# Kernel tuning notes

Measured on AMD Instinct MI355X. Metric: run time of the kernel, lower is better.

Reference implementation:

```python
import jax, jax.numpy as jnp
import numpy as np
from jax import lax

CUT = 20            # voxel grid per side, hard-coded in the torch module
N, P, OP = 32, 8192, 2048


def _w(key, shape, fan_in):
    return jax.random.normal(key, shape, dtype=jnp.float32) * np.float32(1.0 / np.sqrt(fan_in))


def setup_inputs() -> dict:
    key = jax.random.key(0)
    ks = jax.random.split(key, 20)
    inp = {}
    inp["sc"] = jax.random.uniform(ks[0], (N, P, 2), dtype=jnp.float32, minval=-0.5, maxval=0.5)
    inp["oc"] = jax.random.uniform(ks[1], (N, OP, 2), dtype=jnp.float32, minval=-0.5, maxval=0.5)
    inp["pos"] = jax.random.uniform(ks[2], (N, 2), dtype=jnp.float32, minval=-0.5, maxval=0.5)
    # voxel PointNet MLP (1x1 Conv1d == per-point linear)
    inp["mlp_w1"] = _w(ks[3], (128, 2), 2);        inp["mlp_b1"] = jnp.zeros((128,), jnp.float32)
    inp["mlp_w2"] = _w(ks[4], (256, 128), 128);    inp["mlp_b2"] = jnp.zeros((256,), jnp.float32)
    # dense conv pyramid
    inp["conv1_w"] = _w(ks[5], (512, 256, 3, 3), 256 * 9);   inp["conv1_b"] = jnp.zeros((512,), jnp.float32)
    inp["conv2_w"] = _w(ks[6], (1024, 512, 3, 3), 512 * 9);  inp["conv2_b"] = jnp.zeros((1024,), jnp.float32)
    inp["convt_w"] = _w(ks[7], (512, 1024, 2, 2), 1024 * 4); inp["convt_b"] = jnp.zeros((512,), jnp.float32)
    # object set-abstraction (stack of 1x1 Conv1d)
    inp["sa_w1"] = _w(ks[8], (64, 2), 2);          inp["sa_b1"] = jnp.zeros((64,), jnp.float32)
    inp["sa_w2"] = _w(ks[9], (128, 64), 64);       inp["sa_b2"] = jnp.zeros((128,), jnp.float32)
    inp["sa_w3"] = _w(ks[10], (256, 128), 128);    inp["sa_b3"] = jnp.zeros((256,), jnp.float32)
    inp["sa_w4"] = _w(ks[11], (512, 256), 256);    inp["sa_b4"] = jnp.zeros((512,), jnp.float32)
    # per-cell classifier
    inp["cls_w1"] = _w(ks[12], (1024, 1538), 1538); inp["cls_b1"] = jnp.zeros((1024,), jnp.float32)
    inp["cls_w2"] = _w(ks[13], (256, 1024), 1024);  inp["cls_b2"] = jnp.zeros((256,), jnp.float32)
    inp["cls_w3"] = _w(ks[14], (1, 256), 256);      inp["cls_b3"] = jnp.zeros((1,), jnp.float32)
    return inp


def _conv2d(x, w, b):
    y = lax.conv_general_dilated(x, w, (1, 1), ((1, 1), (1, 1)),
                                 dimension_numbers=("NCHW", "OIHW", "NCHW"))
    return y + b[None, :, None, None]


def _maxpool2(x):
    return lax.reduce_window(x, -jnp.inf, lax.max, (1, 1, 2, 2), (1, 1, 2, 2), "VALID")


def reference(sc, oc, pos,
              mlp_w1, mlp_b1, mlp_w2, mlp_b2,
              conv1_w, conv1_b, conv2_w, conv2_b, convt_w, convt_b,
              sa_w1, sa_b1, sa_w2, sa_b2, sa_w3, sa_b3, sa_w4, sa_b4,
              cls_w1, cls_b1, cls_w2, cls_b2, cls_w3, cls_b3):
    n = sc.shape[0]
    # ---- fused voxelization + PointNet + scatter-max (replaces triple loop) ----
    x, y = sc[..., 0], sc[..., 1]
    # torch condition: cut[i] < x <= cut[i+1] on linspace(-0.5, 0.5, 21)
    bi = jnp.clip(jnp.ceil((x + 0.5) * CUT) - 1, 0, CUT - 1).astype(jnp.int32)
    bj = jnp.clip(jnp.ceil((y + 0.5) * CUT) - 1, 0, CUT - 1).astype(jnp.int32)
    valid = (x > -0.5) & (x <= 0.5) & (y > -0.5) & (y <= 0.5)
    ci = -0.5 + (bi.astype(sc.dtype) + 0.5) / CUT   # voxel center x
    cj = -0.5 + (bj.astype(sc.dtype) + 0.5) / CUT   # voxel center y
    pc = jnp.stack([x - ci, y - cj], axis=-1).reshape(-1, 2)        # [n*P, 2]
    h = jax.nn.relu(pc @ mlp_w1.T + mlp_b1)
    feat = jax.nn.relu(h @ mlp_w2.T + mlp_b2)                       # [n*P, 256]
    seg = jnp.where(valid,
                    jnp.arange(n, dtype=jnp.int32)[:, None] * (CUT * CUT) + bi * CUT + bj,
                    n * CUT * CUT).reshape(-1)                      # invalid -> dummy bin
    nseg = n * CUT * CUT + 1
    mx = jax.ops.segment_max(feat, seg, num_segments=nseg)
    cnt = jax.ops.segment_sum(jnp.ones((n * P,), jnp.float32), seg, num_segments=nseg)
    vox = jnp.where(cnt[:, None] > 0, mx, 0.0)[: n * CUT * CUT]     # empty voxels stay 0
    vox = vox.reshape(n, CUT, CUT, 256).transpose(0, 3, 1, 2)       # [n,256,20,20]
    # ---- dense conv pyramid ----
    f1 = _maxpool2(jax.nn.relu(_conv2d(vox, conv1_w, conv1_b)))     # [n,512,10,10]
    f2 = _maxpool2(jax.nn.relu(_conv2d(f1, conv2_w, conv2_b)))      # [n,1024,5,5]
    f3 = lax.conv_transpose(f2, convt_w, (2, 2), "VALID",
                            dimension_numbers=("NCHW", "OIHW", "NCHW"))
    f3 = f3 + convt_b[None, :, None, None]                          # [n,512,10,10]
    scene = jnp.concatenate([f1, f3], axis=1)                       # [n,1024,10,10]
    S = scene.shape[2]
    scene_flat = scene.reshape(n, 1024, S * S)
    # ---- object PointNet (1x1 convs == per-point linears) + global max ----
    obj_c = oc - jnp.mean(oc, axis=1, keepdims=True)                # [n,OP,2]
    g = jax.nn.relu(obj_c @ sa_w1.T + sa_b1)
    g = jax.nn.relu(g @ sa_w2.T + sa_b2)
    g = jax.nn.relu(g @ sa_w3.T + sa_b3)
    g = jax.nn.relu(g @ sa_w4.T + sa_b4)                            # [n,OP,512]
    obj = jnp.max(g, axis=1)                                        # [n,512]
    obj_tiled = jnp.broadcast_to(obj[:, :, None], (n, 512, S * S))
    # ---- relative position grid ----
    c = -0.5 + (jnp.arange(S, dtype=sc.dtype) + 0.5) / S
    rel_x = jnp.broadcast_to(pos[:, 0][:, None, None] - c[None, :, None], (n, S, S))
    rel_y = jnp.broadcast_to(pos[:, 1][:, None, None] - c[None, None, :], (n, S, S))
    rel = jnp.stack([rel_x, rel_y], axis=1).reshape(n, 2, S * S)
    # ---- per-cell classifier ----
    cin = jnp.concatenate([scene_flat, obj_tiled, rel], axis=1).transpose(0, 2, 1)  # [n,100,1538]
    h = jax.nn.relu(cin @ cls_w1.T + cls_b1)
    h = jax.nn.relu(h @ cls_w2.T + cls_b2)
    return h @ cls_w3.T + cls_b3                                    # [n,100,1]
```

## Files before the change

### kernel.cpp

```cpp
#include <hip/hip_runtime.h>

#define NB 32
#define PP 8192
#define OPP 2048

typedef _Float16 f16;
typedef f16 half8 __attribute__((ext_vector_type(8)));
typedef f16 half4 __attribute__((ext_vector_type(4)));
typedef f16 half2v __attribute__((ext_vector_type(2)));
typedef float f32x4 __attribute__((ext_vector_type(4)));

#define MFMA16(a, b, c) __builtin_amdgcn_mfma_f32_16x16x32_f16(a, b, c, 0, 0, 0)

__global__ __launch_bounds__(256) void prepfuse_k(
    const float* __restrict__ mlp_w2, const float* __restrict__ sa_w2,
    const float* __restrict__ sa_w3, const float* __restrict__ sa_w4,
    const float* __restrict__ cls_w2, const float* __restrict__ cls_w1,
    const float* __restrict__ convt_w, const float* __restrict__ conv1_w,
    const float* __restrict__ conv2_w, const float* __restrict__ oc,
    f16* __restrict__ mw2h, f16* __restrict__ saw2h, f16* __restrict__ saw3h,
    f16* __restrict__ saw4h, f16* __restrict__ cw2h, f16* __restrict__ cw1h,
    f16* __restrict__ ctwh, f16* __restrict__ w1h, f16* __restrict__ w2h,
    float* __restrict__ ocm) {
  __shared__ float tile[512 * 9];
  int bb = blockIdx.x, t = threadIdx.x;
  if (bb < 2048) {
    constexpr int B0 = 8192, B1 = B0 + 2048, B2 = B1 + 8192, B3 = B2 + 32768, B4 = B3 + 65536;
    constexpr int C1e = B4 + 524288;
    constexpr int TOT = C1e + 2097152;
    for (int idx = bb * 256 + t; idx < TOT; idx += 2048 * 256) {
      if (idx < B4) {
        const float* in; f16* out; int off;
        if (idx < B0)      { in = mlp_w2; out = mw2h;  off = idx; }
        else if (idx < B1) { in = sa_w2;  out = saw2h; off = idx - B0; }
        else if (idx < B2) { in = sa_w3;  out = saw3h; off = idx - B1; }
        else if (idx < B3) { in = sa_w4;  out = saw4h; off = idx - B2; }
        else               { in = cls_w2; out = cw2h;  off = idx - B3; }
        float4 v = ((const float4*)in)[off];
        half4 h; h.x = (f16)v.x; h.y = (f16)v.y; h.z = (f16)v.z; h.w = (f16)v.w;
        ((half4*)out)[off] = h;
      } else if (idx < C1e) {
        int i = idx - B4;
        int co = i >> 9, k2 = i & 511;
        float2 v = *(const float2*)(cls_w1 + (size_t)co * 1538 + k2 * 2);
        half2v h = {(f16)v.x, (f16)v.y};
        *(half2v*)(cw1h + (size_t)co * 1024 + k2 * 2) = h;
      } else {
        int i = idx - C1e;
        int j = i & 7, l = (i >> 3) & 63, kb = (i >> 9) & 31, nb = i >> 14;
        int n16 = l & 15, quad = l >> 4;
        int np = nb * 16 + n16;
        int k = kb * 32 + quad * 8 + j;
        int p = np >> 9, o = np & 511;
        ctwh[i] = (f16)convt_w[((size_t)o * 1024 + k) * 4 + (3 - p)];
      }
    }
  } else if (bb < 2080) {
    float* sx = tile; float* sy = tile + 256;
    int n = bb - 2048;
    float ax = 0.f, ay = 0.f;
    for (int p = t; p < OPP; p += 256) {
      ax += oc[((size_t)n * OPP + p) * 2 + 0];
      ay += oc[((size_t)n * OPP + p) * 2 + 1];
    }
    sx[t] = ax; sy[t] = ay;
    __syncthreads();
    for (int s = 128; s > 0; s >>= 1) {
      if (t < s) { sx[t] += sx[t + s]; sy[t] += sy[t + s]; }
      __syncthreads();
    }
    if (t == 0) {
      ocm[n * 2 + 0] = sx[0] / (float)OPP;
      ocm[n * 2 + 1] = sy[0] / (float)OPP;
    }
  } else {
    int co, CI, NBB; const float* src0; f16* wf;
    if (bb < 2592) { co = bb - 2080; CI = 256; NBB = 32; src0 = conv1_w; wf = w1h; }
    else           { co = bb - 2592; CI = 512; NBB = 64; src0 = conv2_w; wf = w2h; }
    const float* src = src0 + (size_t)co * CI * 9;
    for (int i = t; i < CI * 9; i += 256) tile[i] = src[i];
    __syncthreads();
    int nb = co >> 4, l16c = co & 15;
    int tot = (CI / 32) * 9 * 4;
    for (int e = t; e < tot; e += 256) {
      int quad = e & 3;
      int kk = (e >> 2) % 9;
      int cic = e / 36;
      half8 v;
#pragma unroll
      for (int j = 0; j < 8; ++j) v[j] = (f16)tile[(cic * 32 + quad * 8 + j) * 9 + kk];
      *(half8*)(wf + ((((size_t)cic * 9 + kk) * NBB + nb) * 64 + quad * 16 + l16c) * 8) = v;
    }
  }
}

__global__ void cvt16_k(const float* __restrict__ in, f16* __restrict__ out, int n4) {
  int idx = blockIdx.x * 256 + threadIdx.x;
  if (idx >= n4) return;
  float4 v = ((const float4*)in)[idx];
  half4 h; h.x = (f16)v.x; h.y = (f16)v.y; h.z = (f16)v.z; h.w = (f16)v.w;
  ((half4*)out)[idx] = h;
}

__global__ __launch_bounds__(256) void pointnet_lds_k(
    const float* __restrict__ sc, const float* __restrict__ w1, const float* __restrict__ b1,
    const f16* __restrict__ w2h, const float* __restrict__ b2, float* __restrict__ voxg) {
  __shared__ float voxl[400 * 33];
  int t = threadIdx.x, lane = t & 63, w = t >> 6;
  int quad = lane >> 4, l16 = lane & 15;
  int b = blockIdx.x;
  int ps = b & 3, cg = (b >> 2) & 7, n = b >> 5;
  half2v w1x2[16], w1y2[16], b12[16];
#pragma unroll
  for (int i = 0; i < 16; ++i) {
    int k0 = (i >> 2) * 32 + quad * 8 + (i & 3) * 2;
    w1x2[i] = (half2v){(f16)w1[k0 * 2], (f16)w1[(k0 + 1) * 2]};
    w1y2[i] = (half2v){(f16)w1[k0 * 2 + 1], (f16)w1[(k0 + 1) * 2 + 1]};
    b12[i]  = (half2v){(f16)b1[k0], (f16)b1[k0 + 1]};
  }
  half8 bf[2][4];
  float bias[2];
#pragma unroll
  for (int nt = 0; nt < 2; ++nt) {
    int ch = cg * 32 + nt * 16 + l16;
    bias[nt] = b2[ch];
#pragma unroll
    for (int ks = 0; ks < 4; ++ks)
      bf[nt][ks] = *(const half8*)(w2h + (size_t)ch * 128 + ks * 32 + quad * 8);
  }
  for (int i = t; i < 400 * 33; i += 256) voxl[i] = 0.0f;
  __syncthreads();
  const half2v z2 = {};
  const float* scp = sc + ((size_t)n * PP + (size_t)ps * 2048) * 2;
  int p0 = w * 16 + l16;
  float2 xyA = *(const float2*)(scp + p0 * 2);
  float2 xyB = *(const float2*)(scp + (p0 + 64) * 2);
  for (int it = 0; it < 16; ++it) {
    float xA = xyA.x, yA = xyA.y, xB = xyB.x, yB = xyB.y;
    if (it < 15) {
      xyA = *(const float2*)(scp + ((it + 1) * 128 + p0) * 2);
      xyB = *(const float2*)(scp + ((it + 1) * 128 + p0 + 64) * 2);
    }
    float bifA = fminf(fmaxf(ceilf((xA + 0.5f) * 20.0f) - 1.0f, 0.0f), 19.0f);
    float bjfA = fminf(fmaxf(ceilf((yA + 0.5f) * 20.0f) - 1.0f, 0.0f), 19.0f);
    bool vA = (xA > -0.5f) && (xA <= 0.5f) && (yA > -0.5f) && (yA <= 0.5f);
    float pxA = xA - (-0.5f + (bifA + 0.5f) * 0.05f);
    float pyA = yA - (-0.5f + (bjfA + 0.5f) * 0.05f);
    int bnA = vA ? ((int)bifA * 20 + (int)bjfA) : -1;
    float bifB = fminf(fmaxf(ceilf((xB + 0.5f) * 20.0f) - 1.0f, 0.0f), 19.0f);
    float bjfB = fminf(fmaxf(ceilf((yB + 0.5f) * 20.0f) - 1.0f, 0.0f), 19.0f);
    bool vB = (xB > -0.5f) && (xB <= 0.5f) && (yB > -0.5f) && (yB <= 0.5f);
    float pxB = xB - (-0.5f + (bifB + 0.5f) * 0.05f);
    float pyB = yB - (-0.5f + (bjfB + 0.5f) * 0.05f);
    int bnB = vB ? ((int)bifB * 20 + (int)bjfB) : -1;
    f16 pxhA = (f16)pxA, pyhA = (f16)pyA, pxhB = (f16)pxB, pyhB = (f16)pyB;
    half2v px2A = (half2v){pxhA, pxhA}, py2A = (half2v){pyhA, pyhA};
    half2v px2B = (half2v){pxhB, pxhB}, py2B = (half2v){pyhB, pyhB};
    f32x4 acc0A = {}, acc1A = {}, acc0B = {}, acc1B = {};
#pragma unroll
    for (int ks = 0; ks < 4; ++ks) {
      half8 afA, afB;
#pragma unroll
      for (int j2 = 0; j2 < 4; ++j2) {
        half2v wx = w1x2[ks * 4 + j2], wy = w1y2[ks * 4 + j2], bb = b12[ks * 4 + j2];
        half2v tA = wx * px2A + (wy * py2A + bb);
        half2v tB = wx * px2B + (wy * py2B + bb);
        reinterpret_cast<half2v*>(&afA)[j2] = __builtin_elementwise_max(tA, z2);
        reinterpret_cast<half2v*>(&afB)[j2] = __builtin_elementwise_max(tB, z2);
      }
      acc0A = MFMA16(afA, bf[0][ks], acc0A);
      acc0B = MFMA16(afB, bf[0][ks], acc0B);
      acc1A = MFMA16(afA, bf[1][ks], acc1A);
      acc1B = MFMA16(afB, bf[1][ks], acc1B);
    }
#pragma unroll
    for (int r = 0; r < 4; ++r) {
      int bnA2 = __shfl(bnA, quad * 4 + r);
      int bnB2 = __shfl(bnB, quad * 4 + r);
      if (bnA2 >= 0) {
        float v0 = fmaxf(acc0A[r] + bias[0], 0.0f);
        float v1 = fmaxf(acc1A[r] + bias[1], 0.0f);
        atomicMax((int*)voxl + bnA2 * 33 + l16, __float_as_int(v0));
        atomicMax((int*)voxl + bnA2 * 33 + 16 + l16, __float_as_int(v1));
      }
      if (bnB2 >= 0) {
        float v0 = fmaxf(acc0B[r] + bias[0], 0.0f);
        float v1 = fmaxf(acc1B[r] + bias[1], 0.0f);
        atomicMax((int*)voxl + bnB2 * 33 + l16, __float_as_int(v0));
        atomicMax((int*)voxl + bnB2 * 33 + 16 + l16, __float_as_int(v1));
      }
    }
  }
  __syncthreads();
  float* vg = voxg + ((size_t)n * 400) * 256 + cg * 32;
  for (int i = t; i < 400 * 32; i += 256) {
    int bin = i >> 5, c = i & 31;
    float v = voxl[bin * 33 + c];
    if (v > 0.0f)
      atomicMax((int*)(vg + (size_t)bin * 256) + c, __float_as_int(v));
  }
}

template <int H, int W, int CI, int CO, int MSPLIT>
__global__ __launch_bounds__(256, 2) void convmfma_k(
    const f16* __restrict__ inh, const f16* __restrict__ wf,
    const float* __restrict__ bias, f16* __restrict__ outh) {
  constexpr int HS = H / MSPLIT;
  constexpr int Mpix = HS * W;
  constexpr int MT = (Mpix + 15) / 16;
  constexpr int PR = HS + 2, PC = W + 2;
  constexpr int NCIC = CI / 32;
  constexpr int COG = CO / 128;
  constexpr int NBB = CO / 16;
  extern __shared__ char smem[];
  f16* Ap = (f16*)smem;
  int b = blockIdx.x;
  int cog = b % COG;
  int ms = (b / COG) % MSPLIT;
  int n = b / (COG * MSPLIT);
  int co0 = cog * 128;
  int r0 = ms * HS;
  int t = threadIdx.x, lane = t & 63, w = t >> 6;
  int quad = lane >> 4, l16 = lane & 15;
  int nb0 = cog * 8 + w * 2;

  int abase[MT];
#pragma unroll
  for (int mi = 0; mi < MT; ++mi) {
    int pl = mi * 16 + l16; if (pl > Mpix - 1) pl = Mpix - 1;
    int y = pl / W, x = pl - y * W;
    abase[mi] = (y * PC + x) * 40 + quad * 8;
  }
  f32x4 acc[MT][2] = {};

  const f16* inbase = inh + (size_t)n * H * W * CI;

  for (int cic = 0; cic < NCIC; ++cic) {
    __syncthreads();
    for (int cell = t; cell < PR * PC; cell += 256) {
      int pr = cell / PC, pc = cell - pr * PC;
      int yin = r0 - 1 + pr, xin = pc - 1;
      uint4 d0 = {0,0,0,0}, d1 = {0,0,0,0}, d2 = {0,0,0,0}, d3 = {0,0,0,0};
      if (yin >= 0 && yin < H && xin >= 0 && xin < W) {
        const uint4* src = (const uint4*)(inbase + ((size_t)yin * W + xin) * CI + cic * 32);
        d0 = src[0]; d1 = src[1]; d2 = src[2]; d3 = src[3];
      }
      uint4* dst = (uint4*)(Ap + cell * 40);
      dst[0] = d0; dst[1] = d1; dst[2] = d2; dst[3] = d3;
    }
    __syncthreads();
    const f16* wfc = wf + (size_t)(cic * 9) * NBB * 512;
#pragma unroll
    for (int ky = 0; ky < 3; ++ky)
#pragma unroll
      for (int kx = 0; kx < 3; ++kx) {
        int kk = ky * 3 + kx;
        half8 bf0 = *(const half8*)(wfc + ((size_t)(kk * NBB + nb0) * 64 + lane) * 8);
        half8 bf1 = *(const half8*)(wfc + ((size_t)(kk * NBB + nb0 + 1) * 64 + lane) * 8);
        int shift = (ky * PC + kx) * 40;
#pragma unroll
        for (int mi = 0; mi < MT; ++mi) {
          half8 af = *(const half8*)(Ap + abase[mi] + shift);
          acc[mi][0] = MFMA16(af, bf0, acc[mi][0]);
          acc[mi][1] = MFMA16(af, bf1, acc[mi][1]);
        }
      }
  }
  int co_w = co0 + w * 32;
  float bv0 = bias[co_w + l16];
  float bv1 = bias[co_w + 16 + l16];
  f16* ob = outh + ((size_t)n * H * W + (size_t)ms * Mpix) * CO;
#pragma unroll
  for (int mi = 0; mi < MT; ++mi) {
#pragma unroll
    for (int r = 0; r < 4; ++r) {
      int p = mi * 16 + quad * 4 + r;
      if (p < Mpix) {
        float v0 = acc[mi][0][r] + bv0; v0 = v0 > 0.f ? v0 : 0.f;
        float v1 = acc[mi][1][r] + bv1; v1 = v1 > 0.f ? v1 : 0.f;
        ob[(size_t)p * CO + co_w + l16] = (f16)v0;
        ob[(size_t)p * CO + co_w + 16 + l16] = (f16)v1;
      }
    }
  }
}

__global__ void pool1_k(const f16* __restrict__ g1, f16* __restrict__ f1h,
                        f16* __restrict__ scnh) {
  int idx = blockIdx.x * 256 + threadIdx.x;
  if (idx >= 32 * 100 * 256) return;
  int c2 = idx & 255, rem = idx >> 8;
  int op = rem % 100, n = rem / 100;
  int py = op / 10, px = op - py * 10;
  const f16* base = g1 + (((size_t)n * 400 + (size_t)(2 * py) * 20 + 2 * px) * 512) + c2 * 2;
  float a0 = (float)base[0],   a1 = (float)base[1];
  float b0 = (float)base[512], b1 = (float)base[513];
  const f16* base2 = base + 20 * 512;
  float c0 = (float)base2[0],   c1 = (float)base2[1];
  float d0 = (float)base2[512], d1 = (float)base2[513];
  union { f16 h[2]; unsigned u; } pk;
  pk.h[0] = (f16)fmaxf(fmaxf(a0, b0), fmaxf(c0, d0));
  pk.h[1] = (f16)fmaxf(fmaxf(a1, b1), fmaxf(c1, d1));
  *(unsigned*)(f1h + ((size_t)n * 100 + op) * 512 + c2 * 2) = pk.u;
  *(unsigned*)(scnh + ((size_t)n * 100 + op) * 1024 + c2 * 2) = pk.u;
}

__global__ void pool2_k(const f16* __restrict__ g2, f16* __restrict__ f2h) {
  int idx = blockIdx.x * 256 + threadIdx.x;
  if (idx >= 32 * 25 * 512) return;
  int c2 = idx & 511, rem = idx >> 9;
  int op = rem % 25, n = rem / 25;
  int py = op / 5, px = op - py * 5;
  const f16* base = g2 + (((size_t)n * 100 + (size_t)(2 * py) * 10 + 2 * px) * 1024) + c2 * 2;
  float a0 = (float)base[0],    a1 = (float)base[1];
  float b0 = (float)base[1024], b1 = (float)base[1025];
  const f16* base2 = base + 10 * 1024;
  float c0 = (float)base2[0],    c1 = (float)base2[1];
  float d0 = (float)base2[1024], d1 = (float)base2[1025];
  f16* o = f2h + ((size_t)n * 25 + op) * 1024 + c2 * 2;
  o[0] = (f16)fmaxf(fmaxf(a0, b0), fmaxf(c0, d0));
  o[1] = (f16)fmaxf(fmaxf(a1, b1), fmaxf(c1, d1));
}

__global__ __launch_bounds__(256, 2) void convt_mfma_k(
    const f16* __restrict__ f2h, const f16* __restrict__ ctwf,
    const float* __restrict__ ctb, f16* __restrict__ scnh) {
  __shared__ f16 act[25 * 1048];
  int b = blockIdx.x;
  int ng = b & 15, n = b >> 4;
  int t = threadIdx.x, lane = t & 63, w = t >> 6;
  int quad = lane >> 4, l16 = lane & 15;
  for (int i = t; i < 25 * 128; i += 256) {
    int row = i >> 7, c8 = i & 127;
    *(half8*)(act + row * 1048 + c8 * 8) =
        *(const half8*)(f2h + ((size_t)n * 25 + row) * 1024 + c8 * 8);
  }
  __syncthreads();
  int r1 = 16 + (l16 > 8 ? 8 : l16);
  f32x4 acc[2][2] = {};
  const f16* wp0 = ctwf + ((size_t)((ng * 8 + w * 2 + 0) * 32) * 64 + lane) * 8;
  const f16* wp1 = ctwf + ((size_t)((ng * 8 + w * 2 + 1) * 32) * 64 + lane) * 8;
#pragma unroll 4
  for (int ks = 0; ks < 32; ++ks) {
    half8 a0 = *(const half8*)(act + l16 * 1048 + ks * 32 + quad * 8);
    half8 a1 = *(const half8*)(act + r1 * 1048 + ks * 32 + quad * 8);
    half8 b0 = *(const half8*)(wp0 + (size_t)ks * 512);
    half8 b1 = *(const half8*)(wp1 + (size_t)ks * 512);
    acc[0][0] = MFMA16(a0, b0, acc[0][0]);
    acc[1][0] = MFMA16(a1, b0, acc[1][0]);
    acc[0][1] = MFMA16(a0, b1, acc[0][1]);
    acc[1][1] = MFMA16(a1, b1, acc[1][1]);
  }
#pragma unroll
  for (int nt = 0; nt < 2; ++nt) {
    int np = ng * 128 + w * 32 + nt * 16 + l16;
    int p = np >> 9, co = np & 511;
    int a = p >> 1, bc = p & 1;
    float bb = ctb[co];
#pragma unroll
    for (int mt = 0; mt < 2; ++mt)
#pragma unroll
      for (int r = 0; r < 4; ++r) {
        int px = mt * 16 + quad * 4 + r;
        if (px < 25) {
          int ph = px / 5, pw = px - ph * 5;
          int opx = (2 * ph + a) * 10 + 2 * pw + bc;
          scnh[((size_t)n * 100 + opx) * 1024 + 512 + co] = (f16)(acc[mt][nt][r] + bb);
        }
      }
  }
}

__global__ __launch_bounds__(256, 2) void sa_mfma_k(
    const float* __restrict__ oc, const float* __restrict__ ocm,
    const float* __restrict__ w1, const float* __restrict__ b1,
    const f16* __restrict__ w2h, const float* __restrict__ b2,
    const f16* __restrict__ w3h, const float* __restrict__ b3,
    const f16* __restrict__ w4h, const float* __restrict__ b4,
    float* __restrict__ obj) {
  __shared__ f16 act1[64 * 72];
  __shared__ f16 act2[64 * 136];
  __shared__ f16 act3[64 * 264];
  __shared__ float pcx[64], pcy[64];
  int b = blockIdx.x;
  int n = b >> 5, pb = (b & 31) * 64;
  int t = threadIdx.x, lane = t & 63, w = t >> 6;
  int quad = lane >> 4, l16 = lane & 15;
  if (t < 64) {
    pcx[t] = oc[((size_t)n * OPP + pb + t) * 2 + 0] - ocm[n * 2 + 0];
    pcy[t] = oc[((size_t)n * OPP + pb + t) * 2 + 1] - ocm[n * 2 + 1];
  }
  __syncthreads();
  {
    int c = t & 63, pg = t >> 6;
    float wx = w1[c * 2], wy = w1[c * 2 + 1], bb = b1[c];
#pragma unroll
    for (int j = 0; j < 16; ++j) {
      int p = pg * 16 + j;
      act1[p * 72 + c] = (f16)fmaxf(fmaf(wx, pcx[p], fmaf(wy, pcy[p], bb)), 0.0f);
    }
  }
  __syncthreads();
  {
    int n0 = w * 32;
    f32x4 acc[4][2] = {};
#pragma unroll
    for (int ks = 0; ks < 2; ++ks) {
      half8 a[4];
#pragma unroll
      for (int mt = 0; mt < 4; ++mt)
        a[mt] = *(const half8*)(act1 + (mt * 16 + l16) * 72 + ks * 32 + quad * 8);
#pragma unroll
      for (int nt = 0; nt < 2; ++nt) {
        half8 bf = *(const half8*)(w2h + (size_t)(n0 + nt * 16 + l16) * 64 + ks * 32 + quad * 8);
#pragma unroll
        for (int mt = 0; mt < 4; ++mt)
          acc[mt][nt] = MFMA16(a[mt], bf, acc[mt][nt]);
      }
    }
#pragma unroll
    for (int nt = 0; nt < 2; ++nt) {
      int col = n0 + nt * 16 + l16;
      float bb = b2[col];
#pragma unroll
      for (int mt = 0; mt < 4; ++mt)
#pragma unroll
        for (int r = 0; r < 4; ++r)
          act2[(mt * 16 + quad * 4 + r) * 136 + col] = (f16)fmaxf(acc[mt][nt][r] + bb, 0.0f);
    }
  }
  __syncthreads();
  {
    int n0 = w * 64;
    f32x4 acc[4][4] = {};
#pragma unroll
    for (int ks = 0; ks < 4; ++ks) {
      half8 a[4];
#pragma unroll
      for (int mt = 0; mt < 4; ++mt)
        a[mt] = *(const half8*)(act2 + (mt * 16 + l16) * 136 + ks * 32 + quad * 8);
#pragma unroll
      for (int nt = 0; nt < 4; ++nt) {
        half8 bf = *(const half8*)(w3h + (size_t)(n0 + nt * 16 + l16) * 128 + ks * 32 + quad * 8);
#pragma unroll
        for (int mt = 0; mt < 4; ++mt)
          acc[mt][nt] = MFMA16(a[mt], bf, acc[mt][nt]);
      }
    }
#pragma unroll
    for (int nt = 0; nt < 4; ++nt) {
      int col = n0 + nt * 16 + l16;
      float bb = b3[col];
#pragma unroll
      for (int mt = 0; mt < 4; ++mt)
#pragma unroll
        for (int r = 0; r < 4; ++r)
          act3[(mt * 16 + quad * 4 + r) * 264 + col] = (f16)fmaxf(acc[mt][nt][r] + bb, 0.0f);
    }
  }
  __syncthreads();
  {
    int n0 = w * 128;
    f32x4 acc[4][8] = {};
#pragma unroll
    for (int ks = 0; ks < 8; ++ks) {
      half8 a[4];
#pragma unroll
      for (int mt = 0; mt < 4; ++mt)
        a[mt] = *(const half8*)(act3 + (mt * 16 + l16) * 264 + ks * 32 + quad * 8);
#pragma unroll
      for (int nt = 0; nt < 8; ++nt) {
        half8 bf = *(const half8*)(w4h + (size_t)(n0 + nt * 16 + l16) * 256 + ks * 32 + quad * 8);
#pragma unroll
        for (int mt = 0; mt < 4; ++mt)
          acc[mt][nt] = MFMA16(a[mt], bf, acc[mt][nt]);
      }
    }
#pragma unroll
    for (int nt = 0; nt < 8; ++nt) {
      int col = n0 + nt * 16 + l16;
      float bb = b4[col];
      float v = 0.0f;
#pragma unroll
      for (int mt = 0; mt < 4; ++mt)
#pragma unroll
        for (int r = 0; r < 4; ++r)
          v = fmaxf(v, acc[mt][nt][r] + bb);
      v = fmaxf(v, 0.0f);
      v = fmaxf(v, __shfl_xor(v, 16));
      v = fmaxf(v, __shfl_xor(v, 32));
      if (quad == 0)
        atomicMax((int*)obj + (size_t)n * 512 + col, __float_as_int(v));
    }
  }
}

__global__ __launch_bounds__(256) void odprep_k(
    const float* __restrict__ obj, const float* __restrict__ w1raw,
    const float* __restrict__ b1, float* __restrict__ odw, float* __restrict__ wab) {
  int co = blockIdx.x;
  int t = threadIdx.x, lane = t & 63, w = t >> 6;
  const float* wr = w1raw + (size_t)co * 1538 + 1024;
  float2 wv[4];
#pragma unroll
  for (int j = 0; j < 4; ++j) wv[j] = *(const float2*)(wr + lane * 8 + j * 2);
  float bb = b1[co];
  for (int i = 0; i < 8; ++i) {
    int n = w * 8 + i;
    const float* ob = obj + (size_t)n * 512 + lane * 8;
    float od = 0.0f;
#pragma unroll
    for (int j = 0; j < 4; ++j) {
      float2 ov = *(const float2*)(ob + j * 2);
      od = fmaf(wv[j].x, ov.x, od);
      od = fmaf(wv[j].y, ov.y, od);
    }
    od += __shfl_xor(od, 1);  od += __shfl_xor(od, 2);
    od += __shfl_xor(od, 4);  od += __shfl_xor(od, 8);
    od += __shfl_xor(od, 16); od += __shfl_xor(od, 32);
    if (lane == 0) odw[(size_t)n * 1024 + co] = od + bb;
  }
  if (t == 0) { wab[co * 2] = wr[512]; wab[co * 2 + 1] = wr[513]; }
}

__global__ __launch_bounds__(256) void cls1_mfma_k(
    const f16* __restrict__ scnh, const float* __restrict__ odw,
    const float* __restrict__ wab, const float* __restrict__ pos,
    const f16* __restrict__ w1h, f16* __restrict__ h1h) {
  __shared__ f16 act[25 * 1032];
  __shared__ float odl[128], wAl[128], wBl[128];
  int b = blockIdx.x;
  int o8 = b & 7, mq = (b >> 3) & 3, n = b >> 5;
  int co0 = o8 * 128, p0 = mq * 25;
  int t = threadIdx.x, lane = t & 63, w = t >> 6;
  int quad = lane >> 4, l16 = lane & 15;
  for (int i = t; i < 25 * 128; i += 256) {
    int row = i >> 7, c8 = i & 127;
    *(half8*)(act + row * 1032 + c8 * 8) =
        *(const half8*)(scnh + ((size_t)n * 100 + p0 + row) * 1024 + c8 * 8);
  }
  if (t < 128) {
    odl[t] = odw[(size_t)n * 1024 + co0 + t];
    float2 ab = *(const float2*)(wab + (size_t)(co0 + t) * 2);
    wAl[t] = ab.x; wBl[t] = ab.y;
  }
  __syncthreads();
  float posx = pos[n * 2 + 0], posy = pos[n * 2 + 1];
  f32x4 acc[2][2];
#pragma unroll
  for (int mt = 0; mt < 2; ++mt)
#pragma unroll
    for (int nt = 0; nt < 2; ++nt) {
      int cl = w * 32 + nt * 16 + l16;
      float od = odl[cl], wA = wAl[cl], wB = wBl[cl];
#pragma unroll
      for (int r = 0; r < 4; ++r) {
        int pl = mt * 16 + quad * 4 + r;
        int px = p0 + (pl < 25 ? pl : 24);
        float relx = posx - (-0.5f + ((px / 10) + 0.5f) * 0.1f);
        float rely = posy - (-0.5f + ((px % 10) + 0.5f) * 0.1f);
        acc[mt][nt][r] = od + relx * wA + rely * wB;
      }
    }
  int gr0 = l16;
  int gr1 = (16 + l16 > 24) ? 24 : 16 + l16;
  const f16* wb0 = w1h + (size_t)(co0 + w * 32 + l16) * 1024 + quad * 8;
  const f16* wb1 = wb0 + (size_t)16 * 1024;
#pragma unroll 4
  for (int kq = 0; kq < 32; ++kq) {
    int k0 = kq * 32;
    half8 bf0 = *(const half8*)(wb0 + k0);
    half8 bf1 = *(const half8*)(wb1 + k0);
    half8 a0 = *(const half8*)(act + gr0 * 1032 + k0 + quad * 8);
    half8 a1 = *(const half8*)(act + gr1 * 1032 + k0 + quad * 8);
    acc[0][0] = MFMA16(a0, bf0, acc[0][0]);
    acc[1][0] = MFMA16(a1, bf0, acc[1][0]);
    acc[0][1] = MFMA16(a0, bf1, acc[0][1]);
    acc[1][1] = MFMA16(a1, bf1, acc[1][1]);
  }
#pragma unroll
  for (int mt = 0; mt < 2; ++mt)
#pragma unroll
    for (int nt = 0; nt < 2; ++nt) {
      int co = co0 + w * 32 + nt * 16 + l16;
#pragma unroll
      for (int r = 0; r < 4; ++r) {
        int pl = mt * 16 + quad * 4 + r;
        if (pl < 25)
          h1h[((size_t)n * 100 + p0 + pl) * 1024 + co] = (f16)fmaxf(acc[mt][nt][r], 0.0f);
      }
    }
}

__global__ __launch_bounds__(256) void cls2_mfma_k(
    const f16* __restrict__ h1h, const f16* __restrict__ w2h16,
    const float* __restrict__ b2, f16* __restrict__ h2h) {
  __shared__ f16 act[25 * 1032];
  int b = blockIdx.x;
  int ng = b & 1, mq = (b >> 1) & 3, n = b >> 3;
  int co0 = ng * 128, p0 = mq * 25;
  int t = threadIdx.x, lane = t & 63, w = t >> 6;
  int quad = lane >> 4, l16 = lane & 15;
  for (int i = t; i < 25 * 128; i += 256) {
    int row = i >> 7, c8 = i & 127;
    *(half8*)(act + row * 1032 + c8 * 8) =
        *(const half8*)(h1h + ((size_t)n * 100 + p0 + row) * 1024 + c8 * 8);
  }
  __syncthreads();
  f32x4 acc[2][2] = {};
  int gr0 = l16;
  int gr1 = (16 + l16 > 24) ? 24 : 16 + l16;
  const f16* wb0 = w2h16 + (size_t)(co0 + w * 32 + l16) * 1024 + quad * 8;
  const f16* wb1 = wb0 + (size_t)16 * 1024;
#pragma unroll 4
  for (int kq = 0; kq < 32; ++kq) {
    int k0 = kq * 32;
    half8 bf0 = *(const half8*)(wb0 + k0);
    half8 bf1 = *(const half8*)(wb1 + k0);
    half8 a0 = *(const half8*)(act + gr0 * 1032 + k0 + quad * 8);
    half8 a1 = *(const half8*)(act + gr1 * 1032 + k0 + quad * 8);
    acc[0][0] = MFMA16(a0, bf0, acc[0][0]);
    acc[1][0] = MFMA16(a1, bf0, acc[1][0]);
    acc[0][1] = MFMA16(a0, bf1, acc[0][1]);
    acc[1][1] = MFMA16(a1, bf1, acc[1][1]);
  }
#pragma unroll
  for (int mt = 0; mt < 2; ++mt)
#pragma unroll
    for (int nt = 0; nt < 2; ++nt) {
      int co = co0 + w * 32 + nt * 16 + l16;
      float bb = b2[co];
#pragma unroll
      for (int r = 0; r < 4; ++r) {
        int pl = mt * 16 + quad * 4 + r;
        if (pl < 25)
          h2h[((size_t)n * 100 + p0 + pl) * 256 + co] = (f16)fmaxf(acc[mt][nt][r] + bb, 0.0f);
      }
    }
}

__global__ void cls3_k(const f16* __restrict__ h2h, const float* __restrict__ w3,
                       const float* __restrict__ b3, float* __restrict__ out) {
  int n = blockIdx.x, t = threadIdx.x;
  if (t < 100) {
    float acc = b3[0];
    const f16* hp = &h2h[((size_t)n * 100 + t) * 256];
    for (int k = 0; k < 256; ++k) acc = fmaf((float)hp[k], w3[k], acc);
    out[n * 100 + t] = acc;
  }
}

extern "C" void kernel_launch(void* const* d_in, const int* in_sizes, int n_in,
                              void* d_out, int out_size, void* d_ws, size_t ws_size,
                              hipStream_t stream) {
  const float* sc      = (const float*)d_in[0];
  const float* oc      = (const float*)d_in[1];
  const float* pos     = (const float*)d_in[2];
  const float* mlp_w1  = (const float*)d_in[3];
  const float* mlp_b1  = (const float*)d_in[4];
  const float* mlp_w2  = (const float*)d_in[5];
  const float* mlp_b2  = (const float*)d_in[6];
  const float* conv1_w = (const float*)d_in[7];
  const float* conv1_b = (const float*)d_in[8];
  const float* conv2_w = (const float*)d_in[9];
  const float* conv2_b = (const float*)d_in[10];
  const float* convt_w = (const float*)d_in[11];
  const float* convt_b = (const float*)d_in[12];
  const float* sa_w1   = (const float*)d_in[13];
  const float* sa_b1   = (const float*)d_in[14];
  const float* sa_w2   = (const float*)d_in[15];
  const float* sa_b2   = (const float*)d_in[16];
  const float* sa_w3   = (const float*)d_in[17];
  const float* sa_b3   = (const float*)d_in[18];
  const float* sa_w4   = (const float*)d_in[19];
  const float* sa_b4   = (const float*)d_in[20];
  const float* cls_w1  = (const float*)d_in[21];
  const float* cls_b1  = (const float*)d_in[22];
  const float* cls_w2  = (const float*)d_in[23];
  const float* cls_b2  = (const float*)d_in[24];
  const float* cls_w3  = (const float*)d_in[25];
  const float* cls_b3  = (const float*)d_in[26];

  float* ws = (float*)d_ws;
  f16*   w1h   = (f16*)ws;
  f16*   w2h   = (f16*)(ws + 589824);
  f16*   mw2h  = (f16*)(ws + 2949120);
  f16*   saw2h = (f16*)(ws + 2965504);
  f16*   saw3h = (f16*)(ws + 2969600);
  f16*   saw4h = (f16*)(ws + 2985984);
  f16*   cw1h  = (f16*)(ws + 3051520);
  f16*   ctwh  = (f16*)(ws + 3575808);
  f16*   cw2h  = (f16*)(ws + 4624384);
  float* obj   = ws + 4870144;
  float* big   = ws + 4886528;
  f16*   voxh  = (f16*)(ws + 8163328);
  f16*   f1h   = (f16*)(ws + 8982528);
  f16*   scnh  = (f16*)(ws + 9801728);
  float* ocm   = ws + 11456512;

  float* voxg  = big;
  f16*   g1buf = (f16*)big;
  f16*   g2buf = (f16*)big;
  f16*   f2h   = voxh;
  f16*   h1h   = w2h;
  f16*   h2h   = scnh;
  float* odw   = big + 2097152;
  float* wab   = big + 2129920;
  float* outp  = (float*)d_out;

  hipMemsetAsync(obj, 0, (size_t)(16384 + 3276800) * 4, stream);
  prepfuse_k<<<3616, 256, 0, stream>>>(mlp_w2, sa_w2, sa_w3, sa_w4, cls_w2, cls_w1,
                                       convt_w, conv1_w, conv2_w, oc,
                                       mw2h, saw2h, saw3h, saw4h, cw2h, cw1h,
                                       ctwh, w1h, w2h, ocm);

  pointnet_lds_k<<<1024, 256, 0, stream>>>(sc, mlp_w1, mlp_b1, mw2h, mlp_b2, voxg);
  cvt16_k<<<3200, 256, 0, stream>>>(voxg, voxh, 819200);

  convmfma_k<20, 20, 256, 512, 4><<<512, 256, 7 * 22 * 80, stream>>>(
      voxh, w1h, conv1_b, g1buf);
  pool1_k<<<3200, 256, 0, stream>>>(g1buf, f1h, scnh);
  convmfma_k<10, 10, 512, 1024, 2><<<512, 256, 7 * 12 * 80, stream>>>(
      f1h, w2h, conv2_b, g2buf);
  pool2_k<<<1600, 256, 0, stream>>>(g2buf, f2h);
  convt_mfma_k<<<512, 256, 0, stream>>>(f2h, ctwh, convt_b, scnh);

  sa_mfma_k<<<1024, 256, 0, stream>>>(oc, ocm, sa_w1, sa_b1, saw2h, sa_b2,
                                      saw3h, sa_b3, saw4h, sa_b4, obj);
  odprep_k<<<1024, 256, 0, stream>>>(obj, cls_w1, cls_b1, odw, wab);

  cls1_mfma_k<<<1024, 256, 0, stream>>>(scnh, odw, wab, pos, cw1h, h1h);
  cls2_mfma_k<<<256, 256, 0, stream>>>(h1h, cw2h, cls_b2, h2h);
  cls3_k<<<32, 128, 0, stream>>>(h2h, cls_w3, cls_b3, outp);
}
```

Baseline: 459.6 us.

## Fuse fp32→fp16 conversion and 2x2 maxpool into conv MFMA kernels

New measurement: 441.1 us (median of 2 runs). 4.0% less time.

```diff
diff --git a/kernel.cpp b/kernel.cpp
--- a/kernel.cpp
+++ b/kernel.cpp
@@ -94,14 +94,6 @@
   }
 }
 
-__global__ void cvt16_k(const float* __restrict__ in, f16* __restrict__ out, int n4) {
-  int idx = blockIdx.x * 256 + threadIdx.x;
-  if (idx >= n4) return;
-  float4 v = ((const float4*)in)[idx];
-  half4 h; h.x = (f16)v.x; h.y = (f16)v.y; h.z = (f16)v.z; h.w = (f16)v.w;
-  ((half4*)out)[idx] = h;
-}
-
 __global__ __launch_bounds__(256) void pointnet_lds_k(
     const float* __restrict__ sc, const float* __restrict__ w1, const float* __restrict__ b1,
     const f16* __restrict__ w2h, const float* __restrict__ b2, float* __restrict__ voxg) {
@@ -201,10 +193,10 @@
   }
 }
 
-template <int H, int W, int CI, int CO, int MSPLIT>
-__global__ __launch_bounds__(256, 2) void convmfma_k(
-    const f16* __restrict__ inh, const f16* __restrict__ wf,
-    const float* __restrict__ bias, f16* __restrict__ outh) {
+template <int H, int W, int CI, int CO, int MSPLIT, bool INF32, bool WR2>
+__global__ __launch_bounds__(256) void convpool_k(
+    const void* __restrict__ inv, const f16* __restrict__ wf,
+    const float* __restrict__ bias, f16* __restrict__ out1, f16* __restrict__ out2) {
   constexpr int HS = H / MSPLIT;
   constexpr int Mpix = HS * W;
   constexpr int MT = (Mpix + 15) / 16;
@@ -212,8 +204,11 @@
   constexpr int NCIC = CI / 32;
   constexpr int COG = CO / 128;
   constexpr int NBB = CO / 16;
+  constexpr int PW = W / 2;
+  constexpr int POPS = (H / 2) * (W / 2);
   extern __shared__ char smem[];
   f16* Ap = (f16*)smem;
+  f16* pb = (f16*)smem;
   int b = blockIdx.x;
   int cog = b % COG;
   int ms = (b / COG) % MSPLIT;
@@ -233,20 +228,35 @@
   }
   f32x4 acc[MT][2] = {};
 
-  const f16* inbase = inh + (size_t)n * H * W * CI;
-
   for (int cic = 0; cic < NCIC; ++cic) {
     __syncthreads();
     for (int cell = t; cell < PR * PC; cell += 256) {
       int pr = cell / PC, pc = cell - pr * PC;
       int yin = r0 - 1 + pr, xin = pc - 1;
-      uint4 d0 = {0,0,0,0}, d1 = {0,0,0,0}, d2 = {0,0,0,0}, d3 = {0,0,0,0};
-      if (yin >= 0 && yin < H && xin >= 0 && xin < W) {
-        const uint4* src = (const uint4*)(inbase + ((size_t)yin * W + xin) * CI + cic * 32);
-        d0 = src[0]; d1 = src[1]; d2 = src[2]; d3 = src[3];
-      }
-      uint4* dst = (uint4*)(Ap + cell * 40);
-      dst[0] = d0; dst[1] = d1; dst[2] = d2; dst[3] = d3;
+      if constexpr (INF32) {
+        half8 v[4] = {};
+        if (yin >= 0 && yin < H && xin >= 0 && xin < W) {
+          const float4* src = (const float4*)((const float*)inv +
+              (size_t)n * H * W * CI + ((size_t)yin * W + xin) * CI + cic * 32);
+#pragma unroll
+          for (int j = 0; j < 4; ++j) {
+            float4 a = src[j * 2], c = src[j * 2 + 1];
+            v[j][0] = (f16)a.x; v[j][1] = (f16)a.y; v[j][2] = (f16)a.z; v[j][3] = (f16)a.w;
+            v[j][4] = (f16)c.x; v[j][5] = (f16)c.y; v[j][6] = (f16)c.z; v[j][7] = (f16)c.w;
+          }
+        }
+        half8* dst = (half8*)(Ap + cell * 40);
+        dst[0] = v[0]; dst[1] = v[1]; dst[2] = v[2]; dst[3] = v[3];
+      } else {
+        uint4 d0 = {0,0,0,0}, d1 = {0,0,0,0}, d2 = {0,0,0,0}, d3 = {0,0,0,0};
+        if (yin >= 0 && yin < H && xin >= 0 && xin < W) {
+          const uint4* src = (const uint4*)((const f16*)inv +
+              (size_t)n * H * W * CI + ((size_t)yin * W + xin) * CI + cic * 32);
+          d0 = src[0]; d1 = src[1]; d2 = src[2]; d3 = src[3];
+        }
+        uint4* dst = (uint4*)(Ap + cell * 40);
+        dst[0] = d0; dst[1] = d1; dst[2] = d2; dst[3] = d3;
+      }
     }
     __syncthreads();
     const f16* wfc = wf + (size_t)(cic * 9) * NBB * 512;
@@ -269,57 +279,36 @@
   int co_w = co0 + w * 32;
   float bv0 = bias[co_w + l16];
   float bv1 = bias[co_w + 16 + l16];
-  f16* ob = outh + ((size_t)n * H * W + (size_t)ms * Mpix) * CO;
-#pragma unroll
-  for (int mi = 0; mi < MT; ++mi) {
+  __syncthreads();
+#pragma unroll
+  for (int mi = 0; mi < MT; ++mi)
 #pragma unroll
     for (int r = 0; r < 4; ++r) {
       int p = mi * 16 + quad * 4 + r;
       if (p < Mpix) {
         float v0 = acc[mi][0][r] + bv0; v0 = v0 > 0.f ? v0 : 0.f;
         float v1 = acc[mi][1][r] + bv1; v1 = v1 > 0.f ? v1 : 0.f;
-        ob[(size_t)p * CO + co_w + l16] = (f16)v0;
-        ob[(size_t)p * CO + co_w + 16 + l16] = (f16)v1;
-      }
-    }
-  }
-}
-
-__global__ void pool1_k(const f16* __restrict__ g1, f16* __restrict__ f1h,
-                        f16* __restrict__ scnh) {
-  int idx = blockIdx.x * 256 + threadIdx.x;
-  if (idx >= 32 * 100 * 256) return;
-  int c2 = idx & 255, rem = idx >> 8;
-  int op = rem % 100, n = rem / 100;
-  int py = op / 10, px = op - py * 10;
-  const f16* base = g1 + (((size_t)n * 400 + (size_t)(2 * py) * 20 + 2 * px) * 512) + c2 * 2;
-  float a0 = (float)base[0],   a1 = (float)base[1];
-  float b0 = (float)base[512], b1 = (float)base[513];
-  const f16* base2 = base + 20 * 512;
-  float c0 = (float)base2[0],   c1 = (float)base2[1];
-  float d0 = (float)base2[512], d1 = (float)base2[513];
-  union { f16 h[2]; unsigned u; } pk;
-  pk.h[0] = (f16)fmaxf(fmaxf(a0, b0), fmaxf(c0, d0));
-  pk.h[1] = (f16)fmaxf(fmaxf(a1, b1), fmaxf(c1, d1));
-  *(unsigned*)(f1h + ((size_t)n * 100 + op) * 512 + c2 * 2) = pk.u;
-  *(unsigned*)(scnh + ((size_t)n * 100 + op) * 1024 + c2 * 2) = pk.u;
-}
-
-__global__ void pool2_k(const f16* __restrict__ g2, f16* __restrict__ f2h) {
-  int idx = blockIdx.x * 256 + threadIdx.x;
-  if (idx >= 32 * 25 * 512) return;
-  int c2 = idx & 511, rem = idx >> 9;
-  int op = rem % 25, n = rem / 25;
-  int py = op / 5, px = op - py * 5;
-  const f16* base = g2 + (((size_t)n * 100 + (size_t)(2 * py) * 10 + 2 * px) * 1024) + c2 * 2;
-  float a0 = (float)base[0],    a1 = (float)base[1];
-  float b0 = (float)base[1024], b1 = (float)base[1025];
-  const f16* base2 = base + 10 * 1024;
-  float c0 = (float)base2[0],    c1 = (float)base2[1];
-  float d0 = (float)base2[1024], d1 = (float)base2[1025];
-  f16* o = f2h + ((size_t)n * 25 + op) * 1024 + c2 * 2;
-  o[0] = (f16)fmaxf(fmaxf(a0, b0), fmaxf(c0, d0));
-  o[1] = (f16)fmaxf(fmaxf(a1, b1), fmaxf(c1, d1));
+        pb[p * 136 + w * 32 + l16] = (f16)v0;
+        pb[p * 136 + w * 32 + 16 + l16] = (f16)v1;
+      }
+    }
+  __syncthreads();
+  for (int i = t; i < PW * 64; i += 256) {
+    int px = i >> 6, c2 = (i & 63) * 2;
+    int b00 = (2 * px) * 136 + c2;
+    int b10 = (W + 2 * px) * 136 + c2;
+    float a0 = fmaxf((float)pb[b00], (float)pb[b00 + 136]);
+    float a1 = fmaxf((float)pb[b00 + 1], (float)pb[b00 + 137]);
+    float c0 = fmaxf((float)pb[b10], (float)pb[b10 + 136]);
+    float c1 = fmaxf((float)pb[b10 + 1], (float)pb[b10 + 137]);
+    union { f16 h[2]; unsigned u; } pk;
+    pk.h[0] = (f16)fmaxf(a0, c0);
+    pk.h[1] = (f16)fmaxf(a1, c1);
+    size_t op = (size_t)n * POPS + ms * PW + px;
+    *(unsigned*)(out1 + op * CO + co0 + c2) = pk.u;
+    if constexpr (WR2)
+      *(unsigned*)(out2 + op * 1024 + co0 + c2) = pk.u;
+  }
 }
 
 __global__ __launch_bounds__(256, 2) void convt_mfma_k(
@@ -699,8 +688,6 @@
   float* ocm   = ws + 11456512;
 
   float* voxg  = big;
-  f16*   g1buf = (f16*)big;
-  f16*   g2buf = (f16*)big;
   f16*   f2h   = voxh;
   f16*   h1h   = w2h;
   f16*   h2h   = scnh;
@@ -715,14 +702,12 @@
                                        ctwh, w1h, w2h, ocm);
 
   pointnet_lds_k<<<1024, 256, 0, stream>>>(sc, mlp_w1, mlp_b1, mw2h, mlp_b2, voxg);
-  cvt16_k<<<3200, 256, 0, stream>>>(voxg, voxh, 819200);
-
-  convmfma_k<20, 20, 256, 512, 4><<<512, 256, 7 * 22 * 80, stream>>>(
-      voxh, w1h, conv1_b, g1buf);
-  pool1_k<<<3200, 256, 0, stream>>>(g1buf, f1h, scnh);
-  convmfma_k<10, 10, 512, 1024, 2><<<512, 256, 7 * 12 * 80, stream>>>(
-      f1h, w2h, conv2_b, g2buf);
-  pool2_k<<<1600, 256, 0, stream>>>(g2buf, f2h);
+
+  convpool_k<20, 20, 256, 512, 10, true, true><<<1280, 256, 10880, stream>>>(
+      voxg, w1h, conv1_b, f1h, scnh);
+  convpool_k<10, 10, 512, 1024, 5, false, false><<<1280, 256, 5440, stream>>>(
+      f1h, w2h, conv2_b, f2h, nullptr);
+
   convt_mfma_k<<<512, 256, 0, stream>>>(f2h, ctwh, convt_b, scnh);
 
   sa_mfma_k<<<1024, 256, 0, stream>>>(oc, ocm, sa_w1, sa_b1, saw2h, sa_b2,
```
